# Kernel optimization log

Measured on AMD Instinct MI355X. Metric: run time of the kernel, lower is better.

Reference implementation:

```python
import jax, jax.numpy as jnp
import numpy as np

B, C, D, H, W = 16, 8, 511, 16, 16
NHEADS = 16
DIM = C * H * W          # 2048 hidden size
SEQ = D + 1              # 512 tokens incl. cls
HEAD_DIM = DIM // NHEADS # 128


def setup_inputs() -> dict:
    key = jax.random.key(0)
    ks = jax.random.split(key, 8)
    s = 0.02  # weight init scale
    return {
        "x": jax.random.normal(ks[0], (B, C, D, H, W), jnp.float32),
        "pos_embedding": jax.random.normal(ks[1], (1, SEQ, DIM), jnp.float32),
        "cls": jax.random.normal(ks[2], (1, 1, DIM), jnp.float32),
        "qkv_w": jax.random.normal(ks[3], (DIM, 3 * DIM), jnp.float32) * s,
        "qkv_b": jnp.zeros((3 * DIM,), jnp.float32),
        "proj_w": jax.random.normal(ks[4], (DIM, DIM), jnp.float32) * s,
        "proj_b": jnp.zeros((DIM,), jnp.float32),
    }


def reference(x, pos_embedding, cls, qkv_w, qkv_b, proj_w, proj_b):
    b = x.shape[0]
    # rearrange 'b c d h w -> b d (c h w)'
    tok = jnp.transpose(x, (0, 2, 1, 3, 4)).reshape(b, D, DIM)
    tok = jnp.concatenate([jnp.broadcast_to(cls, (b, 1, DIM)), tok], axis=1)
    tok = tok + pos_embedding  # (b, SEQ, DIM)
    # qkv projection (dropout probs are 0 -> identity)
    qkv = tok @ qkv_w + qkv_b  # (b, SEQ, 3*DIM)
    qkv = qkv.reshape(b, SEQ, 3, NHEADS, HEAD_DIM).transpose(2, 0, 3, 1, 4)
    q, k, v = qkv[0], qkv[1], qkv[2]  # each (b, nH, SEQ, hd)
    scale = HEAD_DIM ** -0.5
    score = jax.nn.softmax(jnp.einsum('bhqd,bhkd->bhqk', q, k) * scale, axis=-1)
    out = jnp.einsum('bhqk,bhkd->bhqd', score, v)
    out = out.transpose(0, 2, 1, 3).reshape(b, SEQ, DIM)
    out = out @ proj_w + proj_b
    return out[:, 0]  # cls token, (b, DIM)
```

## Files before the change

kernel.cpp:

```cpp
#include <hip/hip_runtime.h>


#define BB   16
#define CC   8
#define DD   511
#define DIM  2048
#define SEQ  512
#define NH   16
#define HD   128
#define W3   6144
#define SCALE 0.08838834764831845f

#define QP_OFF   0
#define G_OFF    131072
#define SCP_OFF  131088
#define SCPSZ    131072
#define RB_OFF   655376
#define UP_OFF   688144
#define AOP_OFF  4882448

typedef __attribute__((ext_vector_type(8))) short short8;
typedef __attribute__((ext_vector_type(4))) float floatx4;

static __device__ inline short bf_hi(float f) {
  return (short)(__float_as_uint(f) >> 16);
}
static __device__ inline float bf_hif(float f) {
  return __uint_as_float(__float_as_uint(f) & 0xffff0000u);
}

__global__ __launch_bounds__(256) void k1_q(
    const float* __restrict__ pos, const float* __restrict__ cls,
    const float* __restrict__ qkv_w, const float* __restrict__ qkv_b,
    float* __restrict__ ws, float* __restrict__ out) {
  int n  = blockIdx.x * 256 + threadIdx.x;
  int dc = blockIdx.y;
  int tid = (blockIdx.x + blockIdx.y * 8) * 256 + threadIdx.x;
  if (tid < 16) ws[G_OFF + tid] = 0.f;
  if (tid < BB * DIM) out[tid] = 0.f;
  int d0 = dc * 32;
  float acc = (dc == 0) ? qkv_b[n] : 0.f;
#pragma unroll 8
  for (int d = d0; d < d0 + 32; ++d) {
    float t0 = cls[d] + pos[d];
    acc += t0 * qkv_w[(size_t)d * W3 + n];
  }
  ws[QP_OFF + dc * DIM + n] = acc;
}

__global__ __launch_bounds__(128) void k2_r(
    const float* __restrict__ qkv_w, const float* __restrict__ pos,
    const float* __restrict__ cls, float* __restrict__ ws) {
  __shared__ float qs[HD];
  int h = blockIdx.y;
  int d = blockIdx.x * 128 + threadIdx.x;
  float qa = 0.f;
#pragma unroll 8
  for (int c = 0; c < 64; ++c)
    qa += ws[QP_OFF + c * DIM + h * HD + threadIdx.x];
  qs[threadIdx.x] = qa;
  __syncthreads();
  const float4* w4 = reinterpret_cast<const float4*>(
      qkv_w + (size_t)d * W3 + DIM + h * HD);
  float acc = 0.f;
#pragma unroll 8
  for (int e4 = 0; e4 < 32; ++e4) {
    float4 w = w4[e4];
    acc += qs[e4*4+0]*w.x + qs[e4*4+1]*w.y + qs[e4*4+2]*w.z + qs[e4*4+3]*w.w;
  }
  float r = acc * SCALE;
  int i = h * DIM + d;
  short* rb = (short*)(ws + RB_OFF);
  rb[i] = bf_hi(r);
  rb[NH * DIM + i] = bf_hi(r - bf_hif(r));
  float g = (cls[d] + pos[d]) * r;
  for (int m = 1; m < 64; m <<= 1) g += __shfl_xor(g, m, 64);
  if ((threadIdx.x & 63) == 0) atomicAdd(&ws[G_OFF + h], g);
}

__global__ __launch_bounds__(256) void k3_scores_mfma(
    const float* __restrict__ x, const float* __restrict__ pos,
    float* __restrict__ ws) {
  int jt2 = blockIdx.x, b = blockIdx.y, ks = blockIdx.z;
  int t = threadIdx.x;
  int w = t >> 6, l = t & 63;
  int jt = jt2 * 4 + w;
  int m16 = l & 15, kg = l >> 4;
  int jrow = 1 + jt * 16 + m16;
  int jc = jrow < SEQ ? jrow : (SEQ - 1);
  const size_t xrow = (size_t)b * CC * DD * 256 + (size_t)(jc - 1) * 256;
  const short* rh = (const short*)(ws + RB_OFF);
  const short* rl = rh + NH * DIM;
  floatx4 acc = {0.f, 0.f, 0.f, 0.f};
#pragma unroll 2
  for (int kk = ks * 16; kk < ks * 16 + 16; ++kk) {
    int d0 = kk * 32 + kg * 8;
    int c = d0 >> 8, doff = d0 & 255;
    const float4* xp = reinterpret_cast<const float4*>(
        x + xrow + (size_t)c * DD * 256 + doff);
    const float4* pp = reinterpret_cast<const float4*>(
        pos + (size_t)jc * DIM + d0);
    float4 xa = xp[0], xb = xp[1];
    float4 pa = pp[0], pb = pp[1];
    float f[8] = {xa.x + pa.x, xa.y + pa.y, xa.z + pa.z, xa.w + pa.w,
                  xb.x + pb.x, xb.y + pb.y, xb.z + pb.z, xb.w + pb.w};
    short8 ahi, alo;
#pragma unroll
    for (int i = 0; i < 8; ++i) {
      ahi[i] = bf_hi(f[i]);
      alo[i] = bf_hi(f[i] - bf_hif(f[i]));
    }
    short8 bhi = *reinterpret_cast<const short8*>(rh + m16 * DIM + d0);
    short8 blo = *reinterpret_cast<const short8*>(rl + m16 * DIM + d0);
    acc = __builtin_amdgcn_mfma_f32_16x16x32_bf16(ahi, bhi, acc, 0, 0, 0);
    acc = __builtin_amdgcn_mfma_f32_16x16x32_bf16(ahi, blo, acc, 0, 0, 0);
    acc = __builtin_amdgcn_mfma_f32_16x16x32_bf16(alo, bhi, acc, 0, 0, 0);
  }
  int h = m16;
#pragma unroll
  for (int reg = 0; reg < 4; ++reg) {
    int row = kg * 4 + reg;
    int j = 1 + jt * 16 + row;
    if (j < SEQ)
      ws[SCP_OFF + (size_t)ks * SCPSZ + (size_t)(b * NH + h) * SEQ + j] =
          acc[reg];
  }
}

__global__ __launch_bounds__(256) void k5_pv(
    const float* __restrict__ x, const float* __restrict__ pos,
    const float* __restrict__ cls, float* __restrict__ ws) {
  int dt = blockIdx.x, b = blockIdx.y, js = blockIdx.z, t = threadIdx.x;
  __shared__ __attribute__((aligned(16))) float pT[64][20];
  int w = t >> 6, l = t & 63;
  for (int rr = 0; rr < 4; ++rr) {
    int h = w * 4 + rr;
    const float* sc0 = ws + SCP_OFF + (size_t)(b * NH + h) * SEQ;
    float gam = ws[G_OFF + h];
    float s[8];
#pragma unroll
    for (int i = 0; i < 8; ++i) {
      int j = i * 64 + l;
      s[i] = sc0[j] + sc0[SCPSZ + j] + sc0[2 * SCPSZ + j] + sc0[3 * SCPSZ + j];
    }
    if (l == 0) s[0] = gam;
    float mx = s[0];
#pragma unroll
    for (int i = 1; i < 8; ++i) mx = fmaxf(mx, s[i]);
    for (int m = 1; m < 64; m <<= 1) mx = fmaxf(mx, __shfl_xor(mx, m, 64));
    float e[8], sum = 0.f;
#pragma unroll
    for (int i = 0; i < 8; ++i) { e[i] = __expf(s[i] - mx); sum += e[i]; }
    for (int m = 1; m < 64; m <<= 1) sum += __shfl_xor(sum, m, 64);
    float inv = 1.f / sum;
    pT[l][h] = e[js] * inv;
  }
  __syncthreads();
  int d = dt * 1024 + t * 4;
  int c = d >> 8, doff = d & 255;
  const float* xcol = x + (size_t)b * CC * DD * 256 + (size_t)c * DD * 256 + doff;
  floatx4 acc[16];
#pragma unroll
  for (int h = 0; h < 16; ++h) acc[h] = (floatx4){0.f, 0.f, 0.f, 0.f};
#pragma unroll 4
  for (int jl = 0; jl < 64; ++jl) {
    int j = js * 64 + jl;
    floatx4 pv = *reinterpret_cast<const floatx4*>(pos + (size_t)j * DIM + d);
    floatx4 xv = (j == 0)
        ? *reinterpret_cast<const floatx4*>(cls + d)
        : *reinterpret_cast<const floatx4*>(xcol + (size_t)(j - 1) * 256);
    floatx4 tok = xv + pv;
#pragma unroll
    for (int h4 = 0; h4 < 4; ++h4) {
      floatx4 p4 = *reinterpret_cast<const floatx4*>(&pT[jl][h4 * 4]);
      acc[h4 * 4 + 0] += p4.x * tok;
      acc[h4 * 4 + 1] += p4.y * tok;
      acc[h4 * 4 + 2] += p4.z * tok;
      acc[h4 * 4 + 3] += p4.w * tok;
    }
  }
  float* ub = ws + UP_OFF + (size_t)(js * 16 + b) * 16 * 2048 + d;
#pragma unroll
  for (int h = 0; h < 16; ++h)
    *reinterpret_cast<floatx4*>(ub + (size_t)h * 2048) = acc[h];
}

__global__ __launch_bounds__(256) void k6_ao(
    const float* __restrict__ qkv_w, const float* __restrict__ qkv_b,
    float* __restrict__ ws) {
  int nt = blockIdx.x, ks = blockIdx.y, t = threadIdx.x;
  int m = nt * 256 + t;
  int h0 = nt * 2;
  __shared__ __attribute__((aligned(16))) float us[2][128][20];
  for (int s = t; s < 4096; s += 256) {
    int dd = s & 127, bb = (s >> 7) & 15, hh = s >> 11;
    float a = 0.f;
#pragma unroll
    for (int js = 0; js < 8; ++js)
      a += ws[UP_OFF + (size_t)(js * 16 + bb) * 16 * 2048 +
              (size_t)(h0 + hh) * 2048 + ks * 128 + dd];
    us[hh][dd][bb] = a;
  }
  __syncthreads();
  int hl = t >> 7;
  float acc[BB];
#pragma unroll
  for (int bb = 0; bb < BB; ++bb) acc[bb] = 0.f;
  const float* wcol = qkv_w + (size_t)(ks * 128) * W3 + 2 * DIM + m;
#pragma unroll 4
  for (int dd = 0; dd < 128; ++dd) {
    float wv = wcol[(size_t)dd * W3];
    floatx4 u0 = *reinterpret_cast<const floatx4*>(&us[hl][dd][0]);
    floatx4 u1 = *reinterpret_cast<const floatx4*>(&us[hl][dd][4]);
    floatx4 u2 = *reinterpret_cast<const floatx4*>(&us[hl][dd][8]);
    floatx4 u3 = *reinterpret_cast<const floatx4*>(&us[hl][dd][12]);
    acc[0]  += u0.x * wv; acc[1]  += u0.y * wv; acc[2]  += u0.z * wv; acc[3]  += u0.w * wv;
    acc[4]  += u1.x * wv; acc[5]  += u1.y * wv; acc[6]  += u1.z * wv; acc[7]  += u1.w * wv;
    acc[8]  += u2.x * wv; acc[9]  += u2.y * wv; acc[10] += u2.z * wv; acc[11] += u2.w * wv;
    acc[12] += u3.x * wv; acc[13] += u3.y * wv; acc[14] += u3.z * wv; acc[15] += u3.w * wv;
  }
  float bias = (ks == 0) ? qkv_b[2 * DIM + m] : 0.f;
#pragma unroll
  for (int bb = 0; bb < BB; ++bb)
    ws[AOP_OFF + (size_t)(ks * 16 + bb) * 2048 + m] = acc[bb] + bias;
}

__global__ __launch_bounds__(256) void k7_out(
    const float* __restrict__ proj_w, const float* __restrict__ proj_b,
    const float* __restrict__ ws, float* __restrict__ out) {
  int nt = blockIdx.x, ms = blockIdx.y, t = threadIdx.x;
  int n = nt * 256 + t;
  int m0 = ms * 128;
  __shared__ __attribute__((aligned(16))) float as[128][20];
  for (int s = t; s < 2048; s += 256) {
    int mm = s & 127, bb = s >> 7;
    float a = 0.f;
#pragma unroll
    for (int ks = 0; ks < 16; ++ks)
      a += ws[AOP_OFF + (size_t)(ks * 16 + bb) * 2048 + m0 + mm];
    as[mm][bb] = a;
  }
  __syncthreads();
  float acc[BB];
#pragma unroll
  for (int bb = 0; bb < BB; ++bb) acc[bb] = 0.f;
  const float* wcol = proj_w + (size_t)m0 * DIM + n;
#pragma unroll 4
  for (int mm = 0; mm < 128; ++mm) {
    float wv = wcol[(size_t)mm * DIM];
    floatx4 a0 = *reinterpret_cast<const floatx4*>(&as[mm][0]);
    floatx4 a1 = *reinterpret_cast<const floatx4*>(&as[mm][4]);
    floatx4 a2 = *reinterpret_cast<const floatx4*>(&as[mm][8]);
    floatx4 a3 = *reinterpret_cast<const floatx4*>(&as[mm][12]);
    acc[0]  += a0.x * wv; acc[1]  += a0.y * wv; acc[2]  += a0.z * wv; acc[3]  += a0.w * wv;
    acc[4]  += a1.x * wv; acc[5]  += a1.y * wv; acc[6]  += a1.z * wv; acc[7]  += a1.w * wv;
    acc[8]  += a2.x * wv; acc[9]  += a2.y * wv; acc[10] += a2.z * wv; acc[11] += a2.w * wv;
    acc[12] += a3.x * wv; acc[13] += a3.y * wv; acc[14] += a3.z * wv; acc[15] += a3.w * wv;
  }
  float bias = (ms == 0) ? proj_b[n] : 0.f;
#pragma unroll
  for (int bb = 0; bb < BB; ++bb)
    atomicAdd(&out[bb * DIM + n], acc[bb] + bias);
}

extern "C" void kernel_launch(void* const* d_in, const int* in_sizes, int n_in,
                              void* d_out, int out_size, void* d_ws, size_t ws_size,
                              hipStream_t stream) {
  const float* x      = (const float*)d_in[0];
  const float* pos    = (const float*)d_in[1];
  const float* cls    = (const float*)d_in[2];
  const float* qkv_w  = (const float*)d_in[3];
  const float* qkv_b  = (const float*)d_in[4];
  const float* proj_w = (const float*)d_in[5];
  const float* proj_b = (const float*)d_in[6];
  float* ws  = (float*)d_ws;
  float* out = (float*)d_out;

  k1_q          <<<dim3(8, 64),    256, 0, stream>>>(pos, cls, qkv_w, qkv_b, ws, out);
  k2_r          <<<dim3(16, 16),   128, 0, stream>>>(qkv_w, pos, cls, ws);
  k3_scores_mfma<<<dim3(8, 16, 4), 256, 0, stream>>>(x, pos, ws);
  k5_pv         <<<dim3(2, 16, 8), 256, 0, stream>>>(x, pos, cls, ws);
  k6_ao         <<<dim3(8, 16),    256, 0, stream>>>(qkv_w, qkv_b, ws);
  k7_out        <<<dim3(8, 16),    256, 0, stream>>>(proj_w, proj_b, ws, out);
}
```

Measured before the change: 259.5 us.

## Split softmax into its own kernel and double grid parallelism of PV/AO/out

Moves the softmax out of k5_pv into a separate k4_softmax kernel that writes normalized probabilities to workspace, so each PV block no longer recomputes softmax for all 16 heads. k5_pv now handles 2 columns per thread across twice as many blocks. k6_ao and k7_out split their reduction dimension into 64-row chunks with twice as many blocks, and k7 sums 32 partials instead of 16. This raises block counts on a GPU with many CUs, at the cost of an extra launch and more partial-sum traffic through workspace.

```diff
diff --git a/kernel.cpp b/kernel.cpp
--- a/kernel.cpp
+++ b/kernel.cpp
@@ -16,11 +16,13 @@
 #define SCP_OFF  131088
 #define SCPSZ    131072
 #define RB_OFF   655376
-#define UP_OFF   688144
-#define AOP_OFF  4882448
+#define PF_OFF   688144
+#define UP_OFF   819216
+#define AOP_OFF  5013520
 
 typedef __attribute__((ext_vector_type(8))) short short8;
 typedef __attribute__((ext_vector_type(4))) float floatx4;
+typedef __attribute__((ext_vector_type(2))) float floatx2;
 
 static __device__ inline short bf_hi(float f) {
   return (short)(__float_as_uint(f) >> 16);
@@ -127,49 +129,55 @@
   }
 }
 
+__global__ __launch_bounds__(64) void k4_softmax(float* __restrict__ ws) {
+  int h = blockIdx.x, b = blockIdx.y, l = threadIdx.x;
+  const float* sc0 = ws + SCP_OFF + (size_t)(b * NH + h) * SEQ;
+  float gam = ws[G_OFF + h];
+  float s[8];
+#pragma unroll
+  for (int i = 0; i < 8; ++i) {
+    int j = i * 64 + l;
+    s[i] = sc0[j] + sc0[SCPSZ + j] + sc0[2 * SCPSZ + j] + sc0[3 * SCPSZ + j];
+  }
+  if (l == 0) s[0] = gam;
+  float mx = s[0];
+#pragma unroll
+  for (int i = 1; i < 8; ++i) mx = fmaxf(mx, s[i]);
+  for (int m = 1; m < 64; m <<= 1) mx = fmaxf(mx, __shfl_xor(mx, m, 64));
+  float e[8], sum = 0.f;
+#pragma unroll
+  for (int i = 0; i < 8; ++i) { e[i] = __expf(s[i] - mx); sum += e[i]; }
+  for (int m = 1; m < 64; m <<= 1) sum += __shfl_xor(sum, m, 64);
+  float inv = 1.f / sum;
+  float* pf = ws + PF_OFF + (size_t)(b * NH + h) * SEQ;
+#pragma unroll
+  for (int i = 0; i < 8; ++i) pf[i * 64 + l] = e[i] * inv;
+}
+
 __global__ __launch_bounds__(256) void k5_pv(
     const float* __restrict__ x, const float* __restrict__ pos,
     const float* __restrict__ cls, float* __restrict__ ws) {
   int dt = blockIdx.x, b = blockIdx.y, js = blockIdx.z, t = threadIdx.x;
   __shared__ __attribute__((aligned(16))) float pT[64][20];
-  int w = t >> 6, l = t & 63;
-  for (int rr = 0; rr < 4; ++rr) {
-    int h = w * 4 + rr;
-    const float* sc0 = ws + SCP_OFF + (size_t)(b * NH + h) * SEQ;
-    float gam = ws[G_OFF + h];
-    float s[8];
-#pragma unroll
-    for (int i = 0; i < 8; ++i) {
-      int j = i * 64 + l;
-      s[i] = sc0[j] + sc0[SCPSZ + j] + sc0[2 * SCPSZ + j] + sc0[3 * SCPSZ + j];
-    }
-    if (l == 0) s[0] = gam;
-    float mx = s[0];
-#pragma unroll
-    for (int i = 1; i < 8; ++i) mx = fmaxf(mx, s[i]);
-    for (int m = 1; m < 64; m <<= 1) mx = fmaxf(mx, __shfl_xor(mx, m, 64));
-    float e[8], sum = 0.f;
-#pragma unroll
-    for (int i = 0; i < 8; ++i) { e[i] = __expf(s[i] - mx); sum += e[i]; }
-    for (int m = 1; m < 64; m <<= 1) sum += __shfl_xor(sum, m, 64);
-    float inv = 1.f / sum;
-    pT[l][h] = e[js] * inv;
-  }
-  __syncthreads();
-  int d = dt * 1024 + t * 4;
+  for (int s = t; s < 1024; s += 256) {
+    int h = s >> 6, jl = s & 63;
+    pT[jl][h] = ws[PF_OFF + (size_t)(b * NH + h) * SEQ + js * 64 + jl];
+  }
+  __syncthreads();
+  int d = dt * 512 + t * 2;
   int c = d >> 8, doff = d & 255;
   const float* xcol = x + (size_t)b * CC * DD * 256 + (size_t)c * DD * 256 + doff;
-  floatx4 acc[16];
-#pragma unroll
-  for (int h = 0; h < 16; ++h) acc[h] = (floatx4){0.f, 0.f, 0.f, 0.f};
+  floatx2 acc[16];
+#pragma unroll
+  for (int h = 0; h < 16; ++h) acc[h] = (floatx2){0.f, 0.f};
 #pragma unroll 4
   for (int jl = 0; jl < 64; ++jl) {
     int j = js * 64 + jl;
-    floatx4 pv = *reinterpret_cast<const floatx4*>(pos + (size_t)j * DIM + d);
-    floatx4 xv = (j == 0)
-        ? *reinterpret_cast<const floatx4*>(cls + d)
-        : *reinterpret_cast<const floatx4*>(xcol + (size_t)(j - 1) * 256);
-    floatx4 tok = xv + pv;
+    floatx2 pv = *reinterpret_cast<const floatx2*>(pos + (size_t)j * DIM + d);
+    floatx2 xv = (j == 0)
+        ? *reinterpret_cast<const floatx2*>(cls + d)
+        : *reinterpret_cast<const floatx2*>(xcol + (size_t)(j - 1) * 256);
+    floatx2 tok = xv + pv;
 #pragma unroll
     for (int h4 = 0; h4 < 4; ++h4) {
       floatx4 p4 = *reinterpret_cast<const floatx4*>(&pT[jl][h4 * 4]);
@@ -182,7 +190,7 @@
   float* ub = ws + UP_OFF + (size_t)(js * 16 + b) * 16 * 2048 + d;
 #pragma unroll
   for (int h = 0; h < 16; ++h)
-    *reinterpret_cast<floatx4*>(ub + (size_t)h * 2048) = acc[h];
+    *reinterpret_cast<floatx2*>(ub + (size_t)h * 2048) = acc[h];
 }
 
 __global__ __launch_bounds__(256) void k6_ao(
@@ -191,14 +199,14 @@
   int nt = blockIdx.x, ks = blockIdx.y, t = threadIdx.x;
   int m = nt * 256 + t;
   int h0 = nt * 2;
-  __shared__ __attribute__((aligned(16))) float us[2][128][20];
-  for (int s = t; s < 4096; s += 256) {
-    int dd = s & 127, bb = (s >> 7) & 15, hh = s >> 11;
+  __shared__ __attribute__((aligned(16))) float us[2][64][20];
+  for (int s = t; s < 2048; s += 256) {
+    int dd = s & 63, bb = (s >> 6) & 15, hh = s >> 10;
     float a = 0.f;
 #pragma unroll
     for (int js = 0; js < 8; ++js)
       a += ws[UP_OFF + (size_t)(js * 16 + bb) * 16 * 2048 +
-              (size_t)(h0 + hh) * 2048 + ks * 128 + dd];
+              (size_t)(h0 + hh) * 2048 + ks * 64 + dd];
     us[hh][dd][bb] = a;
   }
   __syncthreads();
@@ -206,9 +214,9 @@
   float acc[BB];
 #pragma unroll
   for (int bb = 0; bb < BB; ++bb) acc[bb] = 0.f;
-  const float* wcol = qkv_w + (size_t)(ks * 128) * W3 + 2 * DIM + m;
+  const float* wcol = qkv_w + (size_t)(ks * 64) * W3 + 2 * DIM + m;
 #pragma unroll 4
-  for (int dd = 0; dd < 128; ++dd) {
+  for (int dd = 0; dd < 64; ++dd) {
     float wv = wcol[(size_t)dd * W3];
     floatx4 u0 = *reinterpret_cast<const floatx4*>(&us[hl][dd][0]);
     floatx4 u1 = *reinterpret_cast<const floatx4*>(&us[hl][dd][4]);
@@ -230,13 +238,13 @@
     const float* __restrict__ ws, float* __restrict__ out) {
   int nt = blockIdx.x, ms = blockIdx.y, t = threadIdx.x;
   int n = nt * 256 + t;
-  int m0 = ms * 128;
-  __shared__ __attribute__((aligned(16))) float as[128][20];
-  for (int s = t; s < 2048; s += 256) {
-    int mm = s & 127, bb = s >> 7;
+  int m0 = ms * 64;
+  __shared__ __attribute__((aligned(16))) float as[64][20];
+  for (int s = t; s < 1024; s += 256) {
+    int mm = s & 63, bb = s >> 6;
     float a = 0.f;
 #pragma unroll
-    for (int ks = 0; ks < 16; ++ks)
+    for (int ks = 0; ks < 32; ++ks)
       a += ws[AOP_OFF + (size_t)(ks * 16 + bb) * 2048 + m0 + mm];
     as[mm][bb] = a;
   }
@@ -246,7 +254,7 @@
   for (int bb = 0; bb < BB; ++bb) acc[bb] = 0.f;
   const float* wcol = proj_w + (size_t)m0 * DIM + n;
 #pragma unroll 4
-  for (int mm = 0; mm < 128; ++mm) {
+  for (int mm = 0; mm < 64; ++mm) {
     float wv = wcol[(size_t)mm * DIM];
     floatx4 a0 = *reinterpret_cast<const floatx4*>(&as[mm][0]);
     floatx4 a1 = *reinterpret_cast<const floatx4*>(&as[mm][4]);
@@ -279,7 +287,8 @@
   k1_q          <<<dim3(8, 64),    256, 0, stream>>>(pos, cls, qkv_w, qkv_b, ws, out);
   k2_r          <<<dim3(16, 16),   128, 0, stream>>>(qkv_w, pos, cls, ws);
   k3_scores_mfma<<<dim3(8, 16, 4), 256, 0, stream>>>(x, pos, ws);
-  k5_pv         <<<dim3(2, 16, 8), 256, 0, stream>>>(x, pos, cls, ws);
-  k6_ao         <<<dim3(8, 16),    256, 0, stream>>>(qkv_w, qkv_b, ws);
-  k7_out        <<<dim3(8, 16),    256, 0, stream>>>(proj_w, proj_b, ws, out);
-}
+  k4_softmax    <<<dim3(16, 16),    64, 0, stream>>>(ws);
+  k5_pv         <<<dim3(4, 16, 8), 256, 0, stream>>>(x, pos, cls, ws);
+  k6_ao         <<<dim3(8, 32),    256, 0, stream>>>(qkv_w, qkv_b, ws);
+  k7_out        <<<dim3(8, 32),    256, 0, stream>>>(proj_w, proj_b, ws, out);
+}
```

After: 244.8 us. -5.7%, faster.
